# Performance work log

Hardware: AMD Instinct MI355X
Metric: run time of the kernel (lower is better)

## Reference

```python
import jax, jax.numpy as jnp
import numpy as np

N_NODES = 100000
N_EDGES = 3200000
N_FEAT = 512
N_HID = 256
N_CLASS = 40
K_HOPS = 10


def setup_inputs() -> dict:
    key = jax.random.key(0)
    ks = jax.random.split(key, 8)
    feature = jax.random.normal(ks[0], (N_NODES, N_FEAT), dtype=jnp.float32)
    edge_row = jax.random.randint(ks[1], (N_EDGES,), 0, N_NODES, dtype=jnp.int32)
    edge_col = jax.random.randint(ks[2], (N_EDGES,), 0, N_NODES, dtype=jnp.int32)
    edge_weight = jax.random.uniform(ks[3], (N_EDGES,), dtype=jnp.float32)
    W1 = jax.random.normal(ks[4], (N_FEAT, N_HID), dtype=jnp.float32) * (1.0 / np.sqrt(N_FEAT))
    b1 = jnp.zeros((N_HID,), dtype=jnp.float32)
    W2 = jax.random.normal(ks[5], (N_HID, N_CLASS), dtype=jnp.float32) * (1.0 / np.sqrt(N_HID))
    b2 = jnp.zeros((N_CLASS,), dtype=jnp.float32)
    Wa = jax.random.normal(ks[6], (N_CLASS, 1), dtype=jnp.float32) * (1.0 / np.sqrt(N_CLASS))
    ba = jnp.zeros((1,), dtype=jnp.float32)
    return {"feature": feature, "edge_row": edge_row, "edge_col": edge_col,
            "edge_weight": edge_weight, "W1": W1, "b1": b1, "W2": W2, "b2": b2,
            "Wa": Wa, "ba": ba}


def reference(feature, edge_row, edge_col, edge_weight, W1, b1, W2, b2, Wa, ba):
    # eval mode: dropout is identity
    x = jax.nn.relu(feature @ W1 + b1)          # [N, H]
    x = x @ W2 + b2                              # [N, C]
    # k-hop sparse propagation: out[i] = sum_e w_e * x[col_e] for row_e == i
    xs = [x]
    for _ in range(K_HOPS):
        x = jax.ops.segment_sum(edge_weight[:, None] * x[edge_col], edge_row,
                                num_segments=N_NODES)
        xs.append(x)
    xs = jnp.stack(xs, axis=1)                   # [N, K+1, C]
    score = jax.nn.sigmoid(jnp.squeeze(xs @ Wa + ba, -1))  # [N, K+1]
    out = jnp.einsum('nk,nkc->nc', score, xs)    # attention-weighted hop sum
    return jax.nn.log_softmax(out, axis=1)
```

## Files before the change

### kernel.cpp

```cpp
#include <hip/hip_runtime.h>
#include <math.h>

#define N_NODES 100000
#define N_EDGES 3200000
#define N_FEAT  512
#define N_HID   256
#define N_CLASS 40
#define K_HOPS  10

#define CAP        80

#define BIN_SHIFT  11
#define NBIN       49
#define NBIN_PAD   56
#define BINCAP     68000
#define CHUNK1     4096
#define CHUNK2     4096
#define CPB2       17

typedef __attribute__((ext_vector_type(8))) short short8;
typedef __attribute__((ext_vector_type(8))) unsigned short ushort8v;
typedef __attribute__((ext_vector_type(4))) float float4v;
typedef unsigned long long u64;

__device__ inline short f2bf(float f)
{
    union { float f; unsigned u; } v; v.f = f;
    unsigned r = v.u + 0x7FFF + ((v.u >> 16) & 1);
    return (short)(r >> 16);
}

__device__ inline float bf2f(unsigned short u)
{
    union { unsigned u; float f; } v; v.u = (unsigned)u << 16;
    return v.f;
}

__global__ void pack_w1(const float* __restrict__ W1, short* __restrict__ W1p)
{
    const int id = blockIdx.x * 256 + threadIdx.x;
    const int kb = id >> 8, n = id & 255;
    short tmp[32];
#pragma unroll
    for (int kl = 0; kl < 32; ++kl)
        tmp[kl] = f2bf(W1[(size_t)(kb * 32 + kl) * N_HID + n]);
    short8* dst = (short8*)&W1p[id * 32];
#pragma unroll
    for (int j = 0; j < 4; ++j) dst[j] = *(short8*)&tmp[j * 8];
}

__global__ void pack_w2(const float* __restrict__ W2, short* __restrict__ W2p)
{
    const int id = blockIdx.x * 256 + threadIdx.x;
    if (id >= 8 * 48) return;
    const int kb = id / 48, n = id % 48;
    short tmp[32];
#pragma unroll
    for (int kl = 0; kl < 32; ++kl)
        tmp[kl] = (n < N_CLASS) ? f2bf(W2[(size_t)(kb * 32 + kl) * N_CLASS + n]) : (short)0;
    short8* dst = (short8*)&W2p[id * 32];
#pragma unroll
    for (int j = 0; j < 4; ++j) dst[j] = *(short8*)&tmp[j * 8];
}

__global__ __launch_bounds__(256) void mlp_mfma(
    const float* __restrict__ feat, const short* __restrict__ W1p,
    const float* __restrict__ b1, const short* __restrict__ W2p,
    const float* __restrict__ b2, const float* __restrict__ Wa,
    const float* __restrict__ ba,
    unsigned short* __restrict__ x0, float* __restrict__ acc_out)
{
    __shared__ __align__(16) short smem[64 * 264];
    short (*As)[40]  = (short(*)[40])smem;
    short (*Hs)[264] = (short(*)[264])smem;

    const int t    = threadIdx.x;
    const int wave = t >> 6;
    const int lane = t & 63;
    const int q    = lane >> 4;
    const int m    = lane & 15;
    const int n0   = blockIdx.x * 64;
    const int colbase = wave * 64;

    float4v acc[4][4];
#pragma unroll
    for (int i = 0; i < 4; ++i)
#pragma unroll
        for (int j = 0; j < 4; ++j) acc[i][j] = (float4v)0.f;

    for (int kb = 0; kb < 16; ++kb) {
        const int k0 = kb * 32;
        __syncthreads();
        {
            const int r  = t >> 2;
            const int kq = t & 3;
            const int n  = n0 + r;
            float f[8];
            if (n < N_NODES) {
                const float* p = &feat[(size_t)n * N_FEAT + k0 + 8 * kq];
                float4 v0 = *(const float4*)p;
                float4 v1 = *(const float4*)(p + 4);
                f[0]=v0.x; f[1]=v0.y; f[2]=v0.z; f[3]=v0.w;
                f[4]=v1.x; f[5]=v1.y; f[6]=v1.z; f[7]=v1.w;
            } else {
#pragma unroll
                for (int j = 0; j < 8; ++j) f[j] = 0.f;
            }
            short8 st;
#pragma unroll
            for (int j = 0; j < 8; ++j) st[j] = f2bf(f[j]);
            *(short8*)&As[r][8 * kq] = st;
        }
        __syncthreads();

        short8 af[4], bfr[4];
#pragma unroll
        for (int rt = 0; rt < 4; ++rt)
            af[rt] = *(const short8*)&As[rt * 16 + m][q * 8];
#pragma unroll
        for (int ct = 0; ct < 4; ++ct) {
            const int off = (kb * 256 + colbase + ct * 16 + m) * 32 + q * 8;
            bfr[ct] = *(const short8*)&W1p[off];
        }
#pragma unroll
        for (int rt = 0; rt < 4; ++rt)
#pragma unroll
            for (int ct = 0; ct < 4; ++ct)
                acc[rt][ct] = __builtin_amdgcn_mfma_f32_16x16x32_bf16(
                    af[rt], bfr[ct], acc[rt][ct], 0, 0, 0);
    }

    __syncthreads();
#pragma unroll
    for (int ct = 0; ct < 4; ++ct) {
        const int col = colbase + ct * 16 + m;
        const float bias = b1[col];
#pragma unroll
        for (int rt = 0; rt < 4; ++rt) {
            const float4v d = acc[rt][ct];
#pragma unroll
            for (int r = 0; r < 4; ++r) {
                const float hv = fmaxf(d[r] + bias, 0.f);
                Hs[rt * 16 + q * 4 + r][col] = f2bf(hv);
            }
        }
    }
    __syncthreads();

    float4v acc2[3];
#pragma unroll
    for (int ct = 0; ct < 3; ++ct) acc2[ct] = (float4v)0.f;
#pragma unroll
    for (int kb = 0; kb < 8; ++kb) {
        const short8 a2 = *(const short8*)&Hs[wave * 16 + m][kb * 32 + q * 8];
#pragma unroll
        for (int ct = 0; ct < 3; ++ct) {
            const int off = (kb * 48 + ct * 16 + m) * 32 + q * 8;
            const short8 b2f = *(const short8*)&W2p[off];
            acc2[ct] = __builtin_amdgcn_mfma_f32_16x16x32_bf16(a2, b2f, acc2[ct], 0, 0, 0);
        }
    }

    float val[3][4];
#pragma unroll
    for (int ct = 0; ct < 3; ++ct) {
        const int col = ct * 16 + m;
        const bool cok = col < N_CLASS;
        const float bias = cok ? b2[col] : 0.f;
#pragma unroll
        for (int r = 0; r < 4; ++r) val[ct][r] = acc2[ct][r] + bias;
        if (cok) {
#pragma unroll
            for (int r = 0; r < 4; ++r) {
                const int row = n0 + wave * 16 + q * 4 + r;
                if (row < N_NODES)
                    x0[(size_t)row * N_CLASS + col] = (unsigned short)f2bf(val[ct][r]);
            }
        }
    }
    float part[4];
#pragma unroll
    for (int r = 0; r < 4; ++r) {
        float p = 0.f;
#pragma unroll
        for (int ct = 0; ct < 3; ++ct) {
            const int col = ct * 16 + m;
            if (col < N_CLASS) p += val[ct][r] * Wa[col];
        }
        part[r] = p;
    }
#pragma unroll
    for (int o = 1; o <= 8; o <<= 1)
#pragma unroll
        for (int r = 0; r < 4; ++r) part[r] += __shfl_xor(part[r], o);
    const float bb = ba[0];
#pragma unroll
    for (int r = 0; r < 4; ++r) {
        const int row = n0 + wave * 16 + q * 4 + r;
        if (row < N_NODES) {
            const float sc = 1.f / (1.f + expf(-(part[r] + bb)));
#pragma unroll
            for (int ct = 0; ct < 3; ++ct) {
                const int col = ct * 16 + m;
                if (col < N_CLASS)
                    acc_out[(size_t)row * N_CLASS + col] = sc * val[ct][r];
            }
        }
    }
}

__global__ __launch_bounds__(256) void bin_kernel(
    const int* __restrict__ erow, const int* __restrict__ ecol,
    const float* __restrict__ ew, int* __restrict__ bin_cursor,
    u64* __restrict__ bins)
{
    __shared__ __align__(16) u64 recs[CHUNK1];
    __shared__ int hist[NBIN], h2[NBIN], lbase[NBIN], adj[NBIN];

    const int t     = threadIdx.x;
    const int cbase = blockIdx.x * CHUNK1;
    const int e0    = cbase + t * 16;
    const bool has  = e0 < N_EDGES;
    const int chunk_n = min(CHUNK1, N_EDGES - cbase);

    for (int i = t; i < NBIN; i += 256) { hist[i] = 0; h2[i] = 0; }
    __syncthreads();

    int   rows[16], cols[16], w15[16];
    if (has) {
#pragma unroll
        for (int qv = 0; qv < 4; ++qv) {
            const int4   r = *(const int4*)&erow[e0 + qv * 4];
            const int4   c = *(const int4*)&ecol[e0 + qv * 4];
            const float4 w = *(const float4*)&ew[e0 + qv * 4];
            rows[qv*4+0]=r.x; rows[qv*4+1]=r.y; rows[qv*4+2]=r.z; rows[qv*4+3]=r.w;
            cols[qv*4+0]=c.x; cols[qv*4+1]=c.y; cols[qv*4+2]=c.z; cols[qv*4+3]=c.w;
            const float wf[4] = {w.x, w.y, w.z, w.w};
#pragma unroll
            for (int j = 0; j < 4; ++j) {
                int v = (int)(wf[j] * 32767.f + 0.5f);
                w15[qv*4+j] = (v > 32767) ? 32767 : v;
            }
        }
#pragma unroll
        for (int j = 0; j < 16; ++j)
            atomicAdd(&hist[rows[j] >> BIN_SHIFT], 1);
    }
    __syncthreads();

    if (t == 0) {
        int run = 0;
        for (int b = 0; b < NBIN; ++b) { lbase[b] = run; run += hist[b]; }
    }
    __syncthreads();
    if (t < NBIN) {
        const int g = atomicAdd(&bin_cursor[t], hist[t]);
        adj[t] = g - lbase[t];
    }
    __syncthreads();

    if (has) {
#pragma unroll
        for (int j = 0; j < 16; ++j) {
            const int b = rows[j] >> BIN_SHIFT;
            const int p = lbase[b] + atomicAdd(&h2[b], 1);
            recs[p] = ((u64)w15[j] << 34) | ((u64)rows[j] << 17) | (u64)cols[j];
        }
    }
    __syncthreads();

    for (int i = t; i < chunk_n; i += 256) {
        const u64 r   = recs[i];
        const int row = (int)((r >> 17) & 0x1FFFF);
        const int b   = row >> BIN_SHIFT;
        const int di  = adj[b] + i;
        if (di < BINCAP)
            bins[(size_t)b * BINCAP + di] = r;
    }
}

__global__ __launch_bounds__(256) void scatter_bins(
    const int* __restrict__ bin_cursor, const u64* __restrict__ bins,
    int* __restrict__ cnt, unsigned int* __restrict__ ebuck)
{
    const int b = blockIdx.x % NBIN_PAD;
    if (b >= NBIN) return;
    const int chunk = blockIdx.x / NBIN_PAD;
    int n = bin_cursor[b];
    if (n > BINCAP) n = BINCAP;
    const int start = chunk * CHUNK2;
    if (start >= n) return;
    const u64* src = &bins[(size_t)b * BINCAP];

#pragma unroll
    for (int j = 0; j < 16; ++j) {
        const int idx = start + j * 256 + threadIdx.x;
        if (idx < n) {
            const u64 r   = src[idx];
            const int col = (int)(r & 0x1FFFF);
            const int row = (int)((r >> 17) & 0x1FFFF);
            const unsigned rec = ((unsigned)(r >> 34) << 17) | (unsigned)col;
            const int pos = atomicAdd(&cnt[row], 1);
            if (pos < CAP)
                ebuck[(size_t)row * CAP + pos] = rec;
        }
    }
}

__global__ __launch_bounds__(256) void hop_kernel(
    const int* __restrict__ cnt, const unsigned int* __restrict__ ebuck,
    const unsigned short* __restrict__ xin,
    unsigned short* __restrict__ xout, float* __restrict__ acc,
    const float* __restrict__ Wa, const float* __restrict__ ba)
{
    const int lane = threadIdx.x & 63;
    const int row  = blockIdx.x * 4 + (threadIdx.x >> 6);
    if (row >= N_NODES) return;
    const int  slot = lane >> 3;
    const int  l    = lane & 7;
    const bool act  = l < 5;

    int n = cnt[row];
    if (n > CAP) n = CAP;
    const size_t ebase = (size_t)row * CAP;

    unsigned rec_a = (lane < n) ? ebuck[ebase + lane] : 0u;

    float s[8];
#pragma unroll
    for (int j = 0; j < 8; ++j) s[j] = 0.f;

    const int nmain = (n < 64) ? n : 64;
    for (int e = 0; e < nmain; e += 8) {
        const unsigned r = __shfl(rec_a, e + slot);
        const int   col  = (int)(r & 0x1FFFFu);
        const float w    = (float)(r >> 17) * (1.f / 32767.f);
        if (act) {
            const ushort8v v = *(const ushort8v*)&xin[(size_t)col * N_CLASS + l * 8];
#pragma unroll
            for (int j = 0; j < 8; ++j) s[j] += w * bf2f(v[j]);
        }
    }
    for (int e = 64; e < n; e += 8) {
        const int ee = e + slot;
        unsigned r = 0u;
        if (ee < n) r = ebuck[ebase + ee];
        const int   col = (int)(r & 0x1FFFFu);
        const float w   = (float)(r >> 17) * (1.f / 32767.f);
        if (act) {
            const ushort8v v = *(const ushort8v*)&xin[(size_t)col * N_CLASS + l * 8];
#pragma unroll
            for (int j = 0; j < 8; ++j) s[j] += w * bf2f(v[j]);
        }
    }

#pragma unroll
    for (int o = 8; o <= 32; o <<= 1)
#pragma unroll
        for (int j = 0; j < 8; ++j) s[j] += __shfl_xor(s[j], o);

    float tq = 0.f;
    if (act) {
#pragma unroll
        for (int j = 0; j < 8; ++j) tq += s[j] * Wa[l * 8 + j];
    }
#pragma unroll
    for (int o = 1; o <= 4; o <<= 1) tq += __shfl_xor(tq, o);
    const float z  = tq + ba[0];
    const float sc = 1.f / (1.f + expf(-z));

    if (act && slot == 0) {
        ushort8v ov;
#pragma unroll
        for (int j = 0; j < 8; ++j) ov[j] = (unsigned short)f2bf(s[j]);
        *(ushort8v*)&xout[(size_t)row * N_CLASS + l * 8] = ov;

        float4* ap0 = (float4*)&acc[(size_t)row * N_CLASS + l * 8];
        float4 a0 = ap0[0];
        float4 a1 = ap0[1];
        a0.x += sc * s[0]; a0.y += sc * s[1]; a0.z += sc * s[2]; a0.w += sc * s[3];
        a1.x += sc * s[4]; a1.y += sc * s[5]; a1.z += sc * s[6]; a1.w += sc * s[7];
        ap0[0] = a0;
        ap0[1] = a1;
    }
}

__device__ inline float wave_sum(float v)
{
#pragma unroll
    for (int o = 32; o; o >>= 1) v += __shfl_xor(v, o);
    return v;
}

__global__ __launch_bounds__(256) void logsoftmax_kernel(
    const float* __restrict__ acc, float* __restrict__ out)
{
    const int lane = threadIdx.x & 63;
    const int row  = blockIdx.x * 4 + (threadIdx.x >> 6);
    if (row >= N_NODES) return;
    const int  c   = lane;
    const bool act = c < N_CLASS;

    float v = act ? acc[(size_t)row * N_CLASS + c] : -INFINITY;
    float mx = v;
#pragma unroll
    for (int o = 32; o; o >>= 1) mx = fmaxf(mx, __shfl_xor(mx, o));
    const float e = act ? expf(v - mx) : 0.f;
    const float s = wave_sum(e);
    if (act) out[(size_t)row * N_CLASS + c] = v - mx - logf(s);
}

extern "C" void kernel_launch(void* const* d_in, const int* in_sizes, int n_in,
                              void* d_out, int out_size, void* d_ws, size_t ws_size,
                              hipStream_t stream)
{
    (void)in_sizes; (void)n_in; (void)out_size; (void)ws_size;
    const float* feat = (const float*)d_in[0];
    const int*   erow = (const int*)d_in[1];
    const int*   ecol = (const int*)d_in[2];
    const float* ew   = (const float*)d_in[3];
    const float* W1   = (const float*)d_in[4];
    const float* b1   = (const float*)d_in[5];
    const float* W2   = (const float*)d_in[6];
    const float* b2   = (const float*)d_in[7];
    const float* Wa   = (const float*)d_in[8];
    const float* ba   = (const float*)d_in[9];
    float* out = (float*)d_out;

    char* ws = (char*)d_ws;
    size_t off = 0;
    auto take = [&](size_t bytes) -> char* {
        char* p = ws + off;
        off += (bytes + 255) & ~(size_t)255;
        return p;
    };
    unsigned short* xb0 = (unsigned short*)take((size_t)N_NODES * N_CLASS * 2 + 64);
    unsigned short* xb1 = (unsigned short*)take((size_t)N_NODES * N_CLASS * 2 + 64);
    float*        acc   = (float*)take((size_t)N_NODES * N_CLASS * 4);
    int*          cnt   = (int*)take((size_t)N_NODES * 4);
    int*          bcur  = (int*)take((size_t)NBIN_PAD * 4);
    short*        W1p   = (short*)take((size_t)N_FEAT * N_HID * 2);
    short*        W2p   = (short*)take((size_t)N_HID * 48 * 2);
    unsigned int* ebuck = (unsigned int*)take((size_t)N_NODES * CAP * 4);
    u64*          bins  = (u64*)take((size_t)NBIN * BINCAP * 8);

    hipMemsetAsync(cnt, 0, (size_t)N_NODES * 4, stream);
    hipMemsetAsync(bcur, 0, (size_t)NBIN_PAD * 4, stream);

    pack_w1<<<16, 256, 0, stream>>>(W1, W1p);
    pack_w2<<<2, 256, 0, stream>>>(W2, W2p);
    mlp_mfma<<<(N_NODES + 63) / 64, 256, 0, stream>>>(feat, W1p, b1, W2p, b2,
                                                      Wa, ba, xb0, acc);

    const int nchunk1 = (N_EDGES + CHUNK1 - 1) / CHUNK1;
    bin_kernel<<<nchunk1, 256, 0, stream>>>(erow, ecol, ew, bcur, bins);
    scatter_bins<<<NBIN_PAD * CPB2, 256, 0, stream>>>(bcur, bins, cnt, ebuck);

    const unsigned short* xin = xb0;
    unsigned short* xout = xb1;
    for (int k = 0; k < K_HOPS; ++k) {
        hop_kernel<<<N_NODES / 4, 256, 0, stream>>>(cnt, ebuck, xin, xout, acc, Wa, ba);
        unsigned short* tmp = (unsigned short*)xin;
        xin  = xout;
        xout = tmp;
    }

    logsoftmax_kernel<<<N_NODES / 4, 256, 0, stream>>>(acc, out);
}
```

Baseline: 1.174 ms.

## Double-buffer MLP feature tiles, narrow hop lanes, fuse log-softmax into last hop

The MLP kernel now prefetches the next 32-column feature slice into registers and writes it to an alternate shared buffer while the MFMAs for the current slice run, halving the barriers per k-step. The hop kernel switches from 8 edges × 8 bf16 per lane to 4 edges × 4 bf16 per lane (16 lanes per edge, 10 active), which changes gather width and edge-level parallelism. The final hop is templated to compute log-softmax in place, removing the separate logsoftmax launch and one full pass over acc. The narrower 8-byte gathers may issue more load instructions per edge.

```diff
diff --git a/kernel.cpp b/kernel.cpp
--- a/kernel.cpp
+++ b/kernel.cpp
@@ -19,7 +19,7 @@
 #define CPB2       17
 
 typedef __attribute__((ext_vector_type(8))) short short8;
-typedef __attribute__((ext_vector_type(8))) unsigned short ushort8v;
+typedef __attribute__((ext_vector_type(4))) unsigned short ushort4v;
 typedef __attribute__((ext_vector_type(4))) float float4v;
 typedef unsigned long long u64;
 
@@ -71,7 +71,7 @@
     unsigned short* __restrict__ x0, float* __restrict__ acc_out)
 {
     __shared__ __align__(16) short smem[64 * 264];
-    short (*As)[40]  = (short(*)[40])smem;
+    short* Abuf      = smem;
     short (*Hs)[264] = (short(*)[264])smem;
 
     const int t    = threadIdx.x;
@@ -82,41 +82,42 @@
     const int n0   = blockIdx.x * 64;
     const int colbase = wave * 64;
 
+    const int r_st  = t >> 2;
+    const int kq_st = t & 3;
+    const int nrow  = n0 + r_st;
+    const bool rok  = nrow < N_NODES;
+    const float* fp = rok ? &feat[(size_t)nrow * N_FEAT + 8 * kq_st] : feat;
+
     float4v acc[4][4];
 #pragma unroll
     for (int i = 0; i < 4; ++i)
 #pragma unroll
         for (int j = 0; j < 4; ++j) acc[i][j] = (float4v)0.f;
 
+    {
+        float4 c0 = {0.f,0.f,0.f,0.f}, c1 = {0.f,0.f,0.f,0.f};
+        if (rok) { c0 = *(const float4*)fp; c1 = *(const float4*)(fp + 4); }
+        short8 st;
+        st[0]=f2bf(c0.x); st[1]=f2bf(c0.y); st[2]=f2bf(c0.z); st[3]=f2bf(c0.w);
+        st[4]=f2bf(c1.x); st[5]=f2bf(c1.y); st[6]=f2bf(c1.z); st[7]=f2bf(c1.w);
+        *(short8*)&Abuf[t * 8] = st;
+    }
+    __syncthreads();
+
     for (int kb = 0; kb < 16; ++kb) {
-        const int k0 = kb * 32;
-        __syncthreads();
-        {
-            const int r  = t >> 2;
-            const int kq = t & 3;
-            const int n  = n0 + r;
-            float f[8];
-            if (n < N_NODES) {
-                const float* p = &feat[(size_t)n * N_FEAT + k0 + 8 * kq];
-                float4 v0 = *(const float4*)p;
-                float4 v1 = *(const float4*)(p + 4);
-                f[0]=v0.x; f[1]=v0.y; f[2]=v0.z; f[3]=v0.w;
-                f[4]=v1.x; f[5]=v1.y; f[6]=v1.z; f[7]=v1.w;
-            } else {
-#pragma unroll
-                for (int j = 0; j < 8; ++j) f[j] = 0.f;
-            }
-            short8 st;
-#pragma unroll
-            for (int j = 0; j < 8; ++j) st[j] = f2bf(f[j]);
-            *(short8*)&As[r][8 * kq] = st;
-        }
-        __syncthreads();
-
+        float4 nv0 = {0.f,0.f,0.f,0.f}, nv1 = {0.f,0.f,0.f,0.f};
+        const bool have = (kb + 1) < 16;
+        if (have && rok) {
+            const float* np = fp + (size_t)(kb + 1) * 32;
+            nv0 = *(const float4*)np;
+            nv1 = *(const float4*)(np + 4);
+        }
+
+        const short* Ar = &Abuf[(kb & 1) * 2048];
         short8 af[4], bfr[4];
 #pragma unroll
         for (int rt = 0; rt < 4; ++rt)
-            af[rt] = *(const short8*)&As[rt * 16 + m][q * 8];
+            af[rt] = *(const short8*)&Ar[(rt * 16 + m) * 32 + q * 8];
 #pragma unroll
         for (int ct = 0; ct < 4; ++ct) {
             const int off = (kb * 256 + colbase + ct * 16 + m) * 32 + q * 8;
@@ -128,9 +129,16 @@
             for (int ct = 0; ct < 4; ++ct)
                 acc[rt][ct] = __builtin_amdgcn_mfma_f32_16x16x32_bf16(
                     af[rt], bfr[ct], acc[rt][ct], 0, 0, 0);
-    }
-
-    __syncthreads();
+
+        if (have) {
+            short8 st;
+            st[0]=f2bf(nv0.x); st[1]=f2bf(nv0.y); st[2]=f2bf(nv0.z); st[3]=f2bf(nv0.w);
+            st[4]=f2bf(nv1.x); st[5]=f2bf(nv1.y); st[6]=f2bf(nv1.z); st[7]=f2bf(nv1.w);
+            *(short8*)&Abuf[((kb + 1) & 1) * 2048 + t * 8] = st;
+        }
+        __syncthreads();
+    }
+
 #pragma unroll
     for (int ct = 0; ct < 4; ++ct) {
         const int col = colbase + ct * 16 + m;
@@ -307,18 +315,20 @@
     }
 }
 
+template <bool LAST>
 __global__ __launch_bounds__(256) void hop_kernel(
     const int* __restrict__ cnt, const unsigned int* __restrict__ ebuck,
     const unsigned short* __restrict__ xin,
     unsigned short* __restrict__ xout, float* __restrict__ acc,
-    const float* __restrict__ Wa, const float* __restrict__ ba)
+    const float* __restrict__ Wa, const float* __restrict__ ba,
+    float* __restrict__ out)
 {
     const int lane = threadIdx.x & 63;
     const int row  = blockIdx.x * 4 + (threadIdx.x >> 6);
     if (row >= N_NODES) return;
-    const int  slot = lane >> 3;
-    const int  l    = lane & 7;
-    const bool act  = l < 5;
+    const int  slot = lane >> 4;
+    const int  l    = lane & 15;
+    const bool act  = l < 10;
 
     int n = cnt[row];
     if (n > CAP) n = CAP;
@@ -326,88 +336,90 @@
 
     unsigned rec_a = (lane < n) ? ebuck[ebase + lane] : 0u;
 
-    float s[8];
-#pragma unroll
-    for (int j = 0; j < 8; ++j) s[j] = 0.f;
+    float s[4];
+#pragma unroll
+    for (int j = 0; j < 4; ++j) s[j] = 0.f;
 
     const int nmain = (n < 64) ? n : 64;
-    for (int e = 0; e < nmain; e += 8) {
+    for (int e = 0; e < nmain; e += 4) {
         const unsigned r = __shfl(rec_a, e + slot);
         const int   col  = (int)(r & 0x1FFFFu);
         const float w    = (float)(r >> 17) * (1.f / 32767.f);
         if (act) {
-            const ushort8v v = *(const ushort8v*)&xin[(size_t)col * N_CLASS + l * 8];
-#pragma unroll
-            for (int j = 0; j < 8; ++j) s[j] += w * bf2f(v[j]);
-        }
-    }
-    for (int e = 64; e < n; e += 8) {
+            const ushort4v v = *(const ushort4v*)&xin[(size_t)col * N_CLASS + l * 4];
+#pragma unroll
+            for (int j = 0; j < 4; ++j) s[j] += w * bf2f(v[j]);
+        }
+    }
+    for (int e = 64; e < n; e += 4) {
         const int ee = e + slot;
         unsigned r = 0u;
         if (ee < n) r = ebuck[ebase + ee];
         const int   col = (int)(r & 0x1FFFFu);
         const float w   = (float)(r >> 17) * (1.f / 32767.f);
         if (act) {
-            const ushort8v v = *(const ushort8v*)&xin[(size_t)col * N_CLASS + l * 8];
-#pragma unroll
-            for (int j = 0; j < 8; ++j) s[j] += w * bf2f(v[j]);
-        }
-    }
-
-#pragma unroll
-    for (int o = 8; o <= 32; o <<= 1)
-#pragma unroll
-        for (int j = 0; j < 8; ++j) s[j] += __shfl_xor(s[j], o);
+            const ushort4v v = *(const ushort4v*)&xin[(size_t)col * N_CLASS + l * 4];
+#pragma unroll
+            for (int j = 0; j < 4; ++j) s[j] += w * bf2f(v[j]);
+        }
+    }
+
+#pragma unroll
+    for (int j = 0; j < 4; ++j) {
+        s[j] += __shfl_xor(s[j], 16);
+        s[j] += __shfl_xor(s[j], 32);
+    }
 
     float tq = 0.f;
     if (act) {
 #pragma unroll
-        for (int j = 0; j < 8; ++j) tq += s[j] * Wa[l * 8 + j];
-    }
-#pragma unroll
-    for (int o = 1; o <= 4; o <<= 1) tq += __shfl_xor(tq, o);
+        for (int j = 0; j < 4; ++j) tq += s[j] * Wa[l * 4 + j];
+    }
+#pragma unroll
+    for (int o = 1; o <= 8; o <<= 1) tq += __shfl_xor(tq, o);
     const float z  = tq + ba[0];
     const float sc = 1.f / (1.f + expf(-z));
 
-    if (act && slot == 0) {
-        ushort8v ov;
-#pragma unroll
-        for (int j = 0; j < 8; ++j) ov[j] = (unsigned short)f2bf(s[j]);
-        *(ushort8v*)&xout[(size_t)row * N_CLASS + l * 8] = ov;
-
-        float4* ap0 = (float4*)&acc[(size_t)row * N_CLASS + l * 8];
-        float4 a0 = ap0[0];
-        float4 a1 = ap0[1];
-        a0.x += sc * s[0]; a0.y += sc * s[1]; a0.z += sc * s[2]; a0.w += sc * s[3];
-        a1.x += sc * s[4]; a1.y += sc * s[5]; a1.z += sc * s[6]; a1.w += sc * s[7];
-        ap0[0] = a0;
-        ap0[1] = a1;
-    }
-}
-
-__device__ inline float wave_sum(float v)
-{
-#pragma unroll
-    for (int o = 32; o; o >>= 1) v += __shfl_xor(v, o);
-    return v;
-}
-
-__global__ __launch_bounds__(256) void logsoftmax_kernel(
-    const float* __restrict__ acc, float* __restrict__ out)
-{
-    const int lane = threadIdx.x & 63;
-    const int row  = blockIdx.x * 4 + (threadIdx.x >> 6);
-    if (row >= N_NODES) return;
-    const int  c   = lane;
-    const bool act = c < N_CLASS;
-
-    float v = act ? acc[(size_t)row * N_CLASS + c] : -INFINITY;
-    float mx = v;
-#pragma unroll
-    for (int o = 32; o; o >>= 1) mx = fmaxf(mx, __shfl_xor(mx, o));
-    const float e = act ? expf(v - mx) : 0.f;
-    const float s = wave_sum(e);
-    if (act) out[(size_t)row * N_CLASS + c] = v - mx - logf(s);
+    const bool wr = act && slot == 0;
+    if (!LAST) {
+        if (wr) {
+            ushort4v ov;
+#pragma unroll
+            for (int j = 0; j < 4; ++j) ov[j] = (unsigned short)f2bf(s[j]);
+            *(ushort4v*)&xout[(size_t)row * N_CLASS + l * 4] = ov;
+
+            float4* ap = (float4*)&acc[(size_t)row * N_CLASS + l * 4];
+            float4 a = *ap;
+            a.x += sc * s[0]; a.y += sc * s[1];
+            a.z += sc * s[2]; a.w += sc * s[3];
+            *ap = a;
+        }
+    } else {
+        float av[4] = {0.f, 0.f, 0.f, 0.f};
+        float mxl = -INFINITY;
+        if (wr) {
+            const float4 a = *(const float4*)&acc[(size_t)row * N_CLASS + l * 4];
+            av[0] = a.x + sc * s[0]; av[1] = a.y + sc * s[1];
+            av[2] = a.z + sc * s[2]; av[3] = a.w + sc * s[3];
+            mxl = fmaxf(fmaxf(av[0], av[1]), fmaxf(av[2], av[3]));
+        }
+        float mx = mxl;
+#pragma unroll
+        for (int o = 1; o <= 8; o <<= 1) mx = fmaxf(mx, __shfl_xor(mx, o));
+        float se = 0.f;
+        if (wr)
+            se = expf(av[0] - mx) + expf(av[1] - mx) +
+                 expf(av[2] - mx) + expf(av[3] - mx);
+#pragma unroll
+        for (int o = 1; o <= 8; o <<= 1) se += __shfl_xor(se, o);
+        if (wr) {
+            const float ls = logf(se);
+            float4 o4;
+            o4.x = av[0] - mx - ls; o4.y = av[1] - mx - ls;
+            o4.z = av[2] - mx - ls; o4.w = av[3] - mx - ls;
+            *(float4*)&out[(size_t)row * N_CLASS + l * 4] = o4;
+        }
+    }
 }
 
 extern "C" void kernel_launch(void* const* d_in, const int* in_sizes, int n_in,
@@ -458,12 +470,13 @@
 
     const unsigned short* xin = xb0;
     unsigned short* xout = xb1;
-    for (int k = 0; k < K_HOPS; ++k) {
-        hop_kernel<<<N_NODES / 4, 256, 0, stream>>>(cnt, ebuck, xin, xout, acc, Wa, ba);
+    for (int k = 0; k < K_HOPS - 1; ++k) {
+        hop_kernel<false><<<N_NODES / 4, 256, 0, stream>>>(
+            cnt, ebuck, xin, xout, acc, Wa, ba, out);
         unsigned short* tmp = (unsigned short*)xin;
         xin  = xout;
         xout = tmp;
     }
-
-    logsoftmax_kernel<<<N_NODES / 4, 256, 0, stream>>>(acc, out);
-}
+    hop_kernel<true><<<N_NODES / 4, 256, 0, stream>>>(
+        cnt, ebuck, xin, xout, acc, Wa, ba, out);
+}
```

Result: slower. 1.298 ms (+10.6%).
